# Optimization experiments

Hardware: AMD Instinct MI355X
Metric: run time of the kernel (lower is better)

Reference implementation:

```python
import jax, jax.numpy as jnp
import numpy as np
from jax.scipy.linalg import cho_solve

D, A, H, N, T = 64, 8, 256, 16, 128
DT = 0.05
# GPR hyperparameters set_hyperparameter(0.1, 0.1, 0.1): lengthscale, signal std, noise std
L2, SF2, SN2 = 0.1 ** 2, 0.1 ** 2, 0.1 ** 2


def _rbf(t1, t2):
    # t1: (P,), t2: (Q,) -> (P, Q) squared-exponential kernel
    d2 = (t1[:, None] - t2[None, :]) ** 2
    return SF2 * jnp.exp(-0.5 * d2 / L2)


def _gp_predict(t, y, tq):
    # t, y: (N,) training inputs/targets; tq: (T,) query times
    K = _rbf(t, t) + SN2 * jnp.eye(t.shape[0], dtype=t.dtype)
    Ks = _rbf(tq, t)          # (T, N)
    Kss = _rbf(tq, tq)        # (T, T)
    Lc = jnp.linalg.cholesky(K)
    alpha = cho_solve((Lc, True), y)        # (N,)
    V = cho_solve((Lc, True), Ks.T)         # (N, T)
    mu = Ks @ alpha                          # (T,)
    cov = Kss - Ks @ V                       # (T, T)
    return mu, cov


def setup_inputs() -> dict:
    key = jax.random.key(0)
    ks = jax.random.split(key, 8)
    def lin(k, out_d, in_d):
        return (jax.random.normal(k, (out_d, in_d), jnp.float32) / np.sqrt(in_d).astype(np.float32))
    return {
        "x": jax.random.normal(ks[0], (512, D), jnp.float32),
        "a": jax.random.normal(ks[1], (512, A), jnp.float32),
        "da": jax.random.normal(ks[2], (512, A), jnp.float32),
        "W1": lin(ks[3], H, D), "b1": jnp.zeros((H,), jnp.float32),
        "W2": lin(ks[4], H, H), "b2": jnp.zeros((H,), jnp.float32),
        "Wt": lin(ks[5], N, H), "bt": jnp.zeros((N,), jnp.float32),
        "Wa": lin(ks[6], N * A, H), "ba": jnp.zeros((N * A,), jnp.float32),
        "time_array": jnp.arange(1, T + 1, dtype=jnp.float32) * DT,
    }


def reference(x, a, da, W1, b1, W2, b2, Wt, bt, Wa, ba, time_array):
    E = x.shape[0]
    h = jnp.tanh(x @ W1.T + b1)
    h = jnp.tanh(h @ W2.T + b2)
    times = h @ Wt.T + bt                              # (E, N)
    anchors = (h @ Wa.T + ba).reshape(E, A, N)         # (E, A, N)
    ts = jnp.broadcast_to(times[:, None, :], (E, A, N)).reshape(E * A, N)
    ys = anchors.reshape(E * A, N)
    mu, cov = jax.vmap(lambda t, y: _gp_predict(t, y, time_array))(ts, ys)
    return mu.reshape(E, A, T), cov.reshape(E, A, T, T)
```

## Files before the change

### kernel.cpp

```cpp
#include <hip/hip_runtime.h>

#define Ecnt 512
#define Dd 64
#define Aa 8
#define Hh 256
#define Nn 16
#define Tt 128
#define NH 144
#define SF2c 0.01f
#define SN2c 0.01f
#define NEGHALF_INV_L2 (-50.0f)

#define OFF_W1T 0
#define OFF_W2T (OFF_W1T + Dd * Hh)
#define OFF_WHT (OFF_W2T + Hh * Hh)
#define OFF_BH  (OFF_WHT + Hh * NH)
#define WS_FLOATS (OFF_BH + NH)

__global__ void prep(const float* __restrict__ W1, const float* __restrict__ W2,
                     const float* __restrict__ Wt, const float* __restrict__ Wa,
                     const float* __restrict__ bt, const float* __restrict__ ba,
                     float* __restrict__ ws) {
    int id = blockIdx.x * blockDim.x + threadIdx.x;
    if (id < Dd * Hh) {
        int k = id >> 8, o = id & 255;
        ws[OFF_W1T + id] = W1[o * Dd + k];
    } else if (id < OFF_WHT) {
        int r = id - OFF_W2T; int k = r >> 8, o = r & 255;
        ws[id] = W2[o * Hh + k];
    } else if (id < OFF_BH) {
        int r = id - OFF_WHT; int k = r / NH, j = r % NH;
        ws[id] = (j < Nn) ? Wt[j * Hh + k] : Wa[(j - Nn) * Hh + k];
    } else if (id < WS_FLOATS) {
        int j = id - OFF_BH;
        ws[id] = (j < Nn) ? bt[j] : ba[j - Nn];
    }
}

__global__ __launch_bounds__(256, 2) void grp_fused(
    const float* __restrict__ x,
    const float* __restrict__ b1, const float* __restrict__ b2,
    const float* __restrict__ tarr, const float* __restrict__ ws,
    float* __restrict__ out_mu, float* __restrict__ out_cov)
{
    const int e   = blockIdx.x;
    const int tid = threadIdx.x;

    __shared__ float xs[Dd];
    __shared__ float h1s[Hh];
    __shared__ float h2s[Hh];
    __shared__ float tt[Nn];
    __shared__ float tq[Tt];
    __shared__ float yy[Aa][Nn];
    __shared__ float Km[Nn][Nn + 1];
    __shared__ float Lm[Nn][Nn + 1];
    __shared__ float tmpv[Nn];
    __shared__ __align__(16) float Ks[Tt][Nn];
    __shared__ __align__(16) float V[Nn][Tt];
    __shared__ float alpha[Aa][Nn];

    if (tid < Dd) xs[tid] = x[e * Dd + tid];
    if (tid < Tt) tq[tid] = tarr[tid];
    __syncthreads();

    const float* __restrict__ W1T = ws + OFF_W1T;
    const float* __restrict__ W2T = ws + OFF_W2T;
    const float* __restrict__ WHT = ws + OFF_WHT;
    const float* __restrict__ BH  = ws + OFF_BH;

    {
        float acc = b1[tid];
        #pragma unroll 8
        for (int k = 0; k < Dd; ++k) acc += W1T[k * Hh + tid] * xs[k];
        h1s[tid] = tanhf(acc);
    }
    __syncthreads();
    {
        float acc = b2[tid];
        #pragma unroll 8
        for (int k = 0; k < Hh; ++k) acc += W2T[k * Hh + tid] * h1s[k];
        h2s[tid] = tanhf(acc);
    }
    __syncthreads();
    if (tid < NH) {
        float acc = BH[tid];
        #pragma unroll 8
        for (int k = 0; k < Hh; ++k) acc += WHT[k * NH + tid] * h2s[k];
        if (tid < Nn) tt[tid] = acc;
        else { int r = tid - Nn; yy[r >> 4][r & 15] = acc; }
    }
    __syncthreads();

    {
        int i = tid >> 4, j = tid & 15;
        float d = tt[i] - tt[j];
        Km[i][j] = SF2c * __expf(NEGHALF_INV_L2 * d * d) + (i == j ? SN2c : 0.f);
    }
    #pragma unroll
    for (int r = 0; r < 8; ++r) {
        int idx = tid + r * 256;
        int q = idx >> 4, i = idx & 15;
        float d = tq[q] - tt[i];
        Ks[q][i] = SF2c * __expf(NEGHALF_INV_L2 * d * d);
    }
    __syncthreads();

    #pragma unroll
    for (int j = 0; j < Nn; ++j) {
        if (tid >= j && tid < Nn) {
            float s = Km[tid][j];
            #pragma unroll
            for (int k = 0; k < j; ++k) s -= Lm[tid][k] * Lm[j][k];
            tmpv[tid] = s;
        }
        __syncthreads();
        if (tid >= j && tid < Nn) {
            float dj = sqrtf(tmpv[j]);
            Lm[tid][j] = (tid == j) ? dj : tmpv[tid] / dj;
        }
        __syncthreads();
    }

    if (tid < Tt + Aa) {
        float bz[Nn];
        if (tid < Tt) {
            float tqv = tq[tid];
            #pragma unroll
            for (int i = 0; i < Nn; ++i) {
                float d = tqv - tt[i];
                bz[i] = SF2c * __expf(NEGHALF_INV_L2 * d * d);
            }
        } else {
            int a = tid - Tt;
            #pragma unroll
            for (int i = 0; i < Nn; ++i) bz[i] = yy[a][i];
        }
        #pragma unroll
        for (int i = 0; i < Nn; ++i) {
            float s = bz[i];
            for (int k = 0; k < i; ++k) s -= Lm[i][k] * bz[k];
            bz[i] = s / Lm[i][i];
        }
        #pragma unroll
        for (int i = Nn - 1; i >= 0; --i) {
            float s = bz[i];
            for (int k = i + 1; k < Nn; ++k) s -= Lm[k][i] * bz[k];
            bz[i] = s / Lm[i][i];
        }
        if (tid < Tt) {
            #pragma unroll
            for (int i = 0; i < Nn; ++i) V[i][tid] = bz[i];
        } else {
            int a = tid - Tt;
            #pragma unroll
            for (int i = 0; i < Nn; ++i) alpha[a][i] = bz[i];
        }
    }
    __syncthreads();

    if (tid < Tt) {
        float ks[Nn];
        #pragma unroll
        for (int i = 0; i < Nn; ++i) ks[i] = Ks[tid][i];
        size_t mb = (size_t)e * (Aa * Tt) + tid;
        #pragma unroll
        for (int a = 0; a < Aa; ++a) {
            float m = 0.f;
            #pragma unroll
            for (int i = 0; i < Nn; ++i) m += ks[i] * alpha[a][i];
            out_mu[mb + (size_t)a * Tt] = m;
        }
    }

    {
        const int q4 = (tid & 31) * 4;
        const int pg = tid >> 5;
        float vq[Nn][4];
        #pragma unroll
        for (int i = 0; i < Nn; ++i) {
            float4 vv = *(const float4*)&V[i][q4];
            vq[i][0] = vv.x; vq[i][1] = vv.y; vq[i][2] = vv.z; vq[i][3] = vv.w;
        }
        const float tqq0 = tq[q4 + 0], tqq1 = tq[q4 + 1], tqq2 = tq[q4 + 2], tqq3 = tq[q4 + 3];
        float* covb = out_cov + (size_t)e * (Aa * Tt * Tt);
        #pragma unroll
        for (int pp = 0; pp < 16; ++pp) {
            const int p = pg * 16 + pp;
            float ksp[Nn];
            #pragma unroll
            for (int i4 = 0; i4 < 4; ++i4) {
                float4 kv = *(const float4*)&Ks[p][i4 * 4];
                ksp[i4*4+0] = kv.x; ksp[i4*4+1] = kv.y; ksp[i4*4+2] = kv.z; ksp[i4*4+3] = kv.w;
            }
            const float tqp = tq[p];
            float d0 = tqp - tqq0, d1 = tqp - tqq1, d2 = tqp - tqq2, d3 = tqp - tqq3;
            float a0 = SF2c * __expf(NEGHALF_INV_L2 * d0 * d0);
            float a1 = SF2c * __expf(NEGHALF_INV_L2 * d1 * d1);
            float a2 = SF2c * __expf(NEGHALF_INV_L2 * d2 * d2);
            float a3 = SF2c * __expf(NEGHALF_INV_L2 * d3 * d3);
            #pragma unroll
            for (int i = 0; i < Nn; ++i) {
                a0 -= ksp[i] * vq[i][0];
                a1 -= ksp[i] * vq[i][1];
                a2 -= ksp[i] * vq[i][2];
                a3 -= ksp[i] * vq[i][3];
            }
            float4 pk; pk.x = a0; pk.y = a1; pk.z = a2; pk.w = a3;
            const size_t ro = (size_t)p * Tt + q4;
            #pragma unroll
            for (int a = 0; a < Aa; ++a) {
                *(float4*)(covb + (size_t)a * (Tt * Tt) + ro) = pk;
            }
        }
    }
}

extern "C" void kernel_launch(void* const* d_in, const int* in_sizes, int n_in,
                              void* d_out, int out_size, void* d_ws, size_t ws_size,
                              hipStream_t stream) {
    (void)in_sizes; (void)n_in; (void)out_size; (void)ws_size;
    const float* x  = (const float*)d_in[0];
    const float* W1 = (const float*)d_in[3];
    const float* b1 = (const float*)d_in[4];
    const float* W2 = (const float*)d_in[5];
    const float* b2 = (const float*)d_in[6];
    const float* Wt = (const float*)d_in[7];
    const float* bt = (const float*)d_in[8];
    const float* Wa = (const float*)d_in[9];
    const float* ba = (const float*)d_in[10];
    const float* ta = (const float*)d_in[11];
    float* mu  = (float*)d_out;
    float* cov = mu + (size_t)Ecnt * Aa * Tt;
    float* wsf = (float*)d_ws;

    prep<<<(WS_FLOATS + 255) / 256, 256, 0, stream>>>(W1, W2, Wt, Wa, bt, ba, wsf);
    grp_fused<<<Ecnt, 256, 0, stream>>>(x, b1, b2, ta, wsf, mu, cov);
}
```

Baseline: 308.0 us.

## Split covariance output into separate kernel with four blocks per sample

Splits the fused kernel in two. The first kernel runs the MLP and GP solve and writes Ks and V to the workspace. A second kernel uses four blocks per sample, each writing a 32-row chunk of the covariance for all anchors. The aim is to spread the large covariance store (512×8×128×128 floats) across more blocks with higher occupancy, rather than a single block per sample doing it after the serial Cholesky. In exchange it adds a kernel launch and a workspace round-trip for Ks and V, and it removes unroll pragmas on the Cholesky loop.

```diff
diff --git a/kernel.cpp b/kernel.cpp
--- a/kernel.cpp
+++ b/kernel.cpp
@@ -15,7 +15,10 @@
 #define OFF_W2T (OFF_W1T + Dd * Hh)
 #define OFF_WHT (OFF_W2T + Hh * Hh)
 #define OFF_BH  (OFF_WHT + Hh * NH)
-#define WS_FLOATS (OFF_BH + NH)
+#define OFF_TT  (OFF_BH + NH)
+#define OFF_KS  (OFF_TT + Ecnt * Nn)
+#define OFF_V   (OFF_KS + Ecnt * Tt * Nn)
+#define WS_FLOATS (OFF_V + Ecnt * Nn * Tt)
 
 __global__ void prep(const float* __restrict__ W1, const float* __restrict__ W2,
                      const float* __restrict__ Wt, const float* __restrict__ Wa,
@@ -31,17 +34,17 @@
     } else if (id < OFF_BH) {
         int r = id - OFF_WHT; int k = r / NH, j = r % NH;
         ws[id] = (j < Nn) ? Wt[j * Hh + k] : Wa[(j - Nn) * Hh + k];
-    } else if (id < WS_FLOATS) {
+    } else if (id < OFF_TT) {
         int j = id - OFF_BH;
         ws[id] = (j < Nn) ? bt[j] : ba[j - Nn];
     }
 }
 
-__global__ __launch_bounds__(256, 2) void grp_fused(
+__global__ __launch_bounds__(256, 2) void grp_solve(
     const float* __restrict__ x,
     const float* __restrict__ b1, const float* __restrict__ b2,
-    const float* __restrict__ tarr, const float* __restrict__ ws,
-    float* __restrict__ out_mu, float* __restrict__ out_cov)
+    const float* __restrict__ tarr, float* __restrict__ ws,
+    float* __restrict__ out_mu)
 {
     const int e   = blockIdx.x;
     const int tid = threadIdx.x;
@@ -105,11 +108,9 @@
     }
     __syncthreads();
 
-    #pragma unroll
     for (int j = 0; j < Nn; ++j) {
         if (tid >= j && tid < Nn) {
             float s = Km[tid][j];
-            #pragma unroll
             for (int k = 0; k < j; ++k) s -= Lm[tid][k] * Lm[j][k];
             tmpv[tid] = s;
         }
@@ -172,45 +173,79 @@
         }
     }
 
-    {
-        const int q4 = (tid & 31) * 4;
-        const int pg = tid >> 5;
-        float vq[Nn][4];
+    if (tid < Nn) ws[OFF_TT + e * Nn + tid] = tt[tid];
+    {
+        float4* dK = (float4*)(ws + OFF_KS + (size_t)e * (Tt * Nn));
+        const float4* sK = (const float4*)&Ks[0][0];
+        dK[tid] = sK[tid];
+        dK[tid + 256] = sK[tid + 256];
+        float4* dV = (float4*)(ws + OFF_V + (size_t)e * (Nn * Tt));
+        const float4* sV = (const float4*)&V[0][0];
+        dV[tid] = sV[tid];
+        dV[tid + 256] = sV[tid + 256];
+    }
+}
+
+__global__ __launch_bounds__(256, 4) void grp_cov(
+    const float* __restrict__ ws, const float* __restrict__ tarr,
+    float* __restrict__ out_cov)
+{
+    const int b  = blockIdx.x;
+    const int e  = b >> 2;
+    const int ch = b & 3;
+    const int tid = threadIdx.x;
+
+    __shared__ __align__(16) float Vs[Nn][Tt];
+    __shared__ __align__(16) float Ksl[32][Nn];
+    __shared__ float tqs[Tt];
+
+    {
+        const float4* sV = (const float4*)(ws + OFF_V + (size_t)e * (Nn * Tt));
+        float4* dV = (float4*)&Vs[0][0];
+        dV[tid] = sV[tid];
+        dV[tid + 256] = sV[tid + 256];
+        if (tid < 128) {
+            const float4* sK = (const float4*)(ws + OFF_KS + (size_t)e * (Tt * Nn) + (size_t)ch * 32 * Nn);
+            ((float4*)&Ksl[0][0])[tid] = sK[tid];
+        }
+        if (tid < Tt) tqs[tid] = tarr[tid];
+    }
+    __syncthreads();
+
+    const int q4 = (tid & 31) * 4;
+    const int pr = tid >> 5;
+    float vq[Nn][4];
+    #pragma unroll
+    for (int i = 0; i < Nn; ++i) {
+        float4 vv = *(const float4*)&Vs[i][q4];
+        vq[i][0] = vv.x; vq[i][1] = vv.y; vq[i][2] = vv.z; vq[i][3] = vv.w;
+    }
+    const float tqq0 = tqs[q4 + 0], tqq1 = tqs[q4 + 1], tqq2 = tqs[q4 + 2], tqq3 = tqs[q4 + 3];
+    float* covb = out_cov + (size_t)e * (Aa * Tt * Tt);
+
+    #pragma unroll
+    for (int pp = 0; pp < 4; ++pp) {
+        const int lp = pr * 4 + pp;
+        const int p  = ch * 32 + lp;
+        const float tqp = tqs[p];
+        float d0 = tqp - tqq0, d1 = tqp - tqq1, d2 = tqp - tqq2, d3 = tqp - tqq3;
+        float a0 = SF2c * __expf(NEGHALF_INV_L2 * d0 * d0);
+        float a1 = SF2c * __expf(NEGHALF_INV_L2 * d1 * d1);
+        float a2 = SF2c * __expf(NEGHALF_INV_L2 * d2 * d2);
+        float a3 = SF2c * __expf(NEGHALF_INV_L2 * d3 * d3);
         #pragma unroll
         for (int i = 0; i < Nn; ++i) {
-            float4 vv = *(const float4*)&V[i][q4];
-            vq[i][0] = vv.x; vq[i][1] = vv.y; vq[i][2] = vv.z; vq[i][3] = vv.w;
-        }
-        const float tqq0 = tq[q4 + 0], tqq1 = tq[q4 + 1], tqq2 = tq[q4 + 2], tqq3 = tq[q4 + 3];
-        float* covb = out_cov + (size_t)e * (Aa * Tt * Tt);
-        #pragma unroll
-        for (int pp = 0; pp < 16; ++pp) {
-            const int p = pg * 16 + pp;
-            float ksp[Nn];
-            #pragma unroll
-            for (int i4 = 0; i4 < 4; ++i4) {
-                float4 kv = *(const float4*)&Ks[p][i4 * 4];
-                ksp[i4*4+0] = kv.x; ksp[i4*4+1] = kv.y; ksp[i4*4+2] = kv.z; ksp[i4*4+3] = kv.w;
-            }
-            const float tqp = tq[p];
-            float d0 = tqp - tqq0, d1 = tqp - tqq1, d2 = tqp - tqq2, d3 = tqp - tqq3;
-            float a0 = SF2c * __expf(NEGHALF_INV_L2 * d0 * d0);
-            float a1 = SF2c * __expf(NEGHALF_INV_L2 * d1 * d1);
-            float a2 = SF2c * __expf(NEGHALF_INV_L2 * d2 * d2);
-            float a3 = SF2c * __expf(NEGHALF_INV_L2 * d3 * d3);
-            #pragma unroll
-            for (int i = 0; i < Nn; ++i) {
-                a0 -= ksp[i] * vq[i][0];
-                a1 -= ksp[i] * vq[i][1];
-                a2 -= ksp[i] * vq[i][2];
-                a3 -= ksp[i] * vq[i][3];
-            }
-            float4 pk; pk.x = a0; pk.y = a1; pk.z = a2; pk.w = a3;
-            const size_t ro = (size_t)p * Tt + q4;
-            #pragma unroll
-            for (int a = 0; a < Aa; ++a) {
-                *(float4*)(covb + (size_t)a * (Tt * Tt) + ro) = pk;
-            }
+            float ks = Ksl[lp][i];
+            a0 -= ks * vq[i][0];
+            a1 -= ks * vq[i][1];
+            a2 -= ks * vq[i][2];
+            a3 -= ks * vq[i][3];
+        }
+        float4 pk; pk.x = a0; pk.y = a1; pk.z = a2; pk.w = a3;
+        const size_t ro = (size_t)p * Tt + q4;
+        #pragma unroll
+        for (int a = 0; a < Aa; ++a) {
+            *(float4*)(covb + (size_t)a * (Tt * Tt) + ro) = pk;
         }
     }
 }
@@ -233,6 +268,7 @@
     float* cov = mu + (size_t)Ecnt * Aa * Tt;
     float* wsf = (float*)d_ws;
 
-    prep<<<(WS_FLOATS + 255) / 256, 256, 0, stream>>>(W1, W2, Wt, Wa, bt, ba, wsf);
-    grp_fused<<<Ecnt, 256, 0, stream>>>(x, b1, b2, ta, wsf, mu, cov);
-}
+    prep<<<(OFF_TT + 255) / 256, 256, 0, stream>>>(W1, W2, Wt, Wa, bt, ba, wsf);
+    grp_solve<<<Ecnt, 256, 0, stream>>>(x, b1, b2, ta, wsf, mu);
+    grp_cov<<<Ecnt * 4, 256, 0, stream>>>(wsf, ta, cov);
+}
```

Result: slower. 323.3 us (+5.0%).
